# Kernel optimization log

Measured on AMD Instinct MI355X. Metric: run time of the kernel, lower is better.

## Reference

```python
import jax, jax.numpy as jnp
import numpy as np

B, S, D, H = 2, 2048, 1024, 16
HD = D // H                      # 64
NUM_ROPE_DIMS = 2
NF = HD // (2 * NUM_ROPE_DIMS)   # 16 freqs per rope dim -> total HD//2
FFN_H = 4 * D


def householder_matrix(vs):
    """Product of Householder reflections: Q = prod_i (I - 2 v_i v_i^T / ||v_i||^2)."""
    dim = vs.shape[-1]
    def step(Q, v):
        v = v[:, None]
        Q = Q - (2.0 / (jnp.sum(v * v) + 1e-8)) * (v @ (v.T @ Q))
        return Q, None
    Q, _ = jax.lax.scan(step, jnp.eye(dim, dtype=vs.dtype), vs)
    return Q


def rmsnorm(x):
    # torch.nn.RMSNorm(eps=None) uses dtype eps, no affine
    return x * jax.lax.rsqrt(jnp.mean(x * x, axis=-1, keepdims=True) + jnp.finfo(x.dtype).eps)


def setup_inputs() -> dict:
    key = jax.random.key(0)
    ks = jax.random.split(key, 8)
    x = jax.random.normal(ks[0], (B, S, D), jnp.float32)
    mask = jnp.tril(jnp.ones((S, S), dtype=bool))          # causal block mask
    qkv_w = jax.random.normal(ks[1], (3 * D, D), jnp.float32) * 0.02
    out_w = jax.random.normal(ks[2], (D, D), jnp.float32) * 0.02
    gate_w = jax.random.normal(ks[3], (D, D), jnp.float32) * 0.02
    gate_b = jnp.zeros((D,), jnp.float32)
    w12 = jax.random.normal(ks[4], (2 * FFN_H, D), jnp.float32) * 0.02
    w3 = jax.random.normal(ks[5], (D, FFN_H), jnp.float32) * 0.02
    hh_vs = jax.random.normal(ks[6], (HD // 2, HD), jnp.float32) * 0.02
    inv_freq = 1.0 / (10000.0 ** (jnp.arange(NF, dtype=jnp.float32) / NF))
    pos = jnp.arange(S, dtype=jnp.float32)
    rope_pos = jnp.stack([pos, pos], axis=-1)              # [S, num_rope_dims]
    return dict(x=x, mask=mask, qkv_w=qkv_w, out_w=out_w, gate_w=gate_w,
                gate_b=gate_b, w12=w12, w3=w3, hh_vs=hh_vs,
                inv_freq=inv_freq, rope_pos=rope_pos)


def reference(x, mask, qkv_w, out_w, gate_w, gate_b, w12, w3, hh_vs, inv_freq, rope_pos):
    Bs, Ss, Ds = x.shape
    resid = x
    xn = rmsnorm(x)
    qkv = xn @ qkv_w.T                                      # [B,S,3D]
    q, k, v = jnp.split(qkv, 3, axis=-1)
    q = q.reshape(Bs, Ss, H, HD).transpose(0, 2, 1, 3)      # [B,H,S,HD]
    k = k.reshape(Bs, Ss, H, HD).transpose(0, 2, 1, 3)
    v = v.reshape(Bs, Ss, H, HD).transpose(0, 2, 1, 3)

    # RnRoPE: rotate into canonical basis, apply RoPE, rotate back
    Q = householder_matrix(hh_vs)                           # [HD,HD]
    q = q @ Q.T
    k = k @ Q.T
    # geo_state.scale = 1.0
    full = jnp.einsum('sd,f->sdf', rope_pos, inv_freq).reshape(Ss, -1)  # [S, HD//2]
    half = HD // 2
    full = full[:, :half]
    emb = jnp.concatenate([full, full], axis=-1)            # [S, HD]
    cos, sin = jnp.cos(emb), jnp.sin(emb)

    def rot(t):
        t1, t2 = jnp.split(t, 2, axis=-1)
        return t * cos + jnp.concatenate([-t2, t1], axis=-1) * sin

    q = rot(q) @ Q
    k = rot(k) @ Q

    # block-masked attention (flex_attention default scale = 1/sqrt(HD))
    scores = jnp.einsum('bhsd,bhtd->bhst', q, k) / jnp.sqrt(jnp.asarray(HD, x.dtype))
    scores = jnp.where(mask, scores, -jnp.inf)
    attn = jax.nn.softmax(scores, axis=-1)
    o = jnp.einsum('bhst,bhtd->bhsd', attn, v)
    o = o.transpose(0, 2, 1, 3).reshape(Bs, Ss, Ds)
    o = o @ out_w.T
    gate = jax.nn.sigmoid(o @ gate_w.T + gate_b)
    x = resid + o * gate

    # SwiGLU FFN
    resid2 = x
    xn2 = rmsnorm(x)
    x12 = xn2 @ w12.T
    x1, x2 = jnp.split(x12, 2, axis=-1)
    ffn = (jax.nn.silu(x1) * x2) @ w3.T
    return resid2 + ffn
```

## Files before the change

kernel.cpp:

```cpp
#include <hip/hip_runtime.h>
#include <hip/hip_bf16.h>
#include <math.h>

constexpr int Bc = 2, Sc = 2048, Dc = 1024, Hc = 16, HDc = 64;
constexpr int D3 = 3 * Dc;

typedef __bf16 bf16x8 __attribute__((ext_vector_type(8)));
typedef float f32x4 __attribute__((ext_vector_type(4)));

__device__ __forceinline__ void gll16(const void* g, void* l) {
  __builtin_amdgcn_global_load_lds((const __attribute__((address_space(1))) unsigned int*)g,
                                   (__attribute__((address_space(3))) unsigned int*)l,
                                   16, 0, 0);
}

__device__ __forceinline__ unsigned short f2bf(float v) {
  __hip_bfloat16 h = __float2bfloat16(v);
  return *(unsigned short*)&h;
}
__device__ __forceinline__ float b2f(unsigned short u) {
  unsigned v = ((unsigned)u) << 16;
  return __uint_as_float(v);
}

#define SBAR() asm volatile("s_barrier" ::: "memory")

__global__ __launch_bounds__(256) void f2b_kernel(const float* __restrict__ in,
                                                  unsigned short* __restrict__ out) {
  int i = blockIdx.x * 256 + threadIdx.x;
  float4 v = ((const float4*)in)[i];
  ushort4 o;
  o.x = f2bf(v.x); o.y = f2bf(v.y); o.z = f2bf(v.z); o.w = f2bf(v.w);
  ((ushort4*)out)[i] = o;
}

__global__ __launch_bounds__(256) void w12i_kernel(const float* __restrict__ in,
                                                   unsigned short* __restrict__ out) {
  int r = blockIdx.x;
  int g = r >> 5, u = r & 31;
  int src = ((u < 16) ? 0 : 4096) + g * 16 + (u & 15);
  float4 v = ((const float4*)(in + (size_t)src * 1024))[threadIdx.x];
  ushort4 o;
  o.x = f2bf(v.x); o.y = f2bf(v.y); o.z = f2bf(v.z); o.w = f2bf(v.w);
  ((ushort4*)(out + (size_t)r * 1024))[threadIdx.x] = o;
}

__global__ __launch_bounds__(256) void rmsnorm_bf16_kernel(const float* __restrict__ in,
                                                           unsigned short* __restrict__ out) {
  int row = blockIdx.x;
  const float4* x4 = (const float4*)(in + (size_t)row * Dc);
  float4 v = x4[threadIdx.x];
  float s = v.x * v.x + v.y * v.y + v.z * v.z + v.w * v.w;
#pragma unroll
  for (int off = 1; off < 64; off <<= 1) s += __shfl_xor(s, off);
  __shared__ float wsum[4];
  if ((threadIdx.x & 63) == 0) wsum[threadIdx.x >> 6] = s;
  __syncthreads();
  float tot = wsum[0] + wsum[1] + wsum[2] + wsum[3];
  float r = rsqrtf(tot * (1.0f / Dc) + 1.1920928955078125e-07f);
  ushort4 o;
  o.x = f2bf(v.x * r); o.y = f2bf(v.y * r); o.z = f2bf(v.z * r); o.w = f2bf(v.w * r);
  ((ushort4*)(out + (size_t)row * Dc))[threadIdx.x] = o;
}

__global__ __launch_bounds__(64) void hh_kernel(const float* __restrict__ vs,
                                                float* __restrict__ Qout) {
  __shared__ float Qm[64][65];
  __shared__ float vsh[64];
  int t = threadIdx.x;
  for (int i = 0; i < 64; ++i) Qm[i][t] = (i == t) ? 1.0f : 0.0f;
  for (int it = 0; it < 32; ++it) {
    __syncthreads();
    vsh[t] = vs[it * 64 + t];
    __syncthreads();
    float nv = 0.0f;
    for (int i = 0; i < 64; ++i) nv += vsh[i] * vsh[i];
    float c = 2.0f / (nv + 1e-8f);
    float wj = 0.0f;
    for (int i = 0; i < 64; ++i) wj += vsh[i] * Qm[i][t];
    for (int i = 0; i < 64; ++i) Qm[i][t] -= c * vsh[i] * wj;
  }
  __syncthreads();
  for (int i = 0; i < 64; ++i) Qout[i * 64 + t] = Qm[i][t];
}

__global__ __launch_bounds__(256) void wqk_kernel(const float* __restrict__ W,
                                                  const float* __restrict__ Qm,
                                                  unsigned short* __restrict__ out) {
  int n = blockIdx.x;
  int r = n & 63;
  int base = n & ~63;
  int t = threadIdx.x;
  float a0 = 0, a1 = 0, a2 = 0, a3 = 0;
  const float4* Wp = (const float4*)(W + (size_t)base * 1024) + t;
#pragma unroll 8
  for (int e = 0; e < 64; ++e) {
    float q = Qm[r * 64 + e];
    float4 wv = Wp[(size_t)e * 256];
    a0 += q * wv.x; a1 += q * wv.y; a2 += q * wv.z; a3 += q * wv.w;
  }
  float sc = (n < 1024) ? 0.18033688f : 1.0f;
  ushort4 o;
  o.x = f2bf(a0 * sc); o.y = f2bf(a1 * sc); o.z = f2bf(a2 * sc); o.w = f2bf(a3 * sc);
  ((ushort4*)(out + (size_t)n * 1024))[t] = o;
}

__global__ __launch_bounds__(256) void rtab_kernel(const float* __restrict__ rope_pos,
                                                   const float* __restrict__ inv_freq,
                                                   float2* __restrict__ tab) {
  int id = blockIdx.x * 256 + threadIdx.x;
  int s = id >> 5, d = id & 31;
  float pos = rope_pos[s * 2 + (d >> 4)];
  float emb = pos * inv_freq[d & 15];
  tab[id] = make_float2(cosf(emb), sinf(emb));
}

__global__ __launch_bounds__(256) void rope_kernel(const unsigned short* __restrict__ qkv,
                                                   const float2* __restrict__ tab,
                                                   unsigned short* __restrict__ qb,
                                                   unsigned short* __restrict__ kb) {
  int t = threadIdx.x;
  int gid = blockIdx.x * 64 + (t >> 2);
  int sub = t & 3;
  int h = gid & 15;
  int which = (gid >> 4) & 1;
  int tok = gid >> 5;
  int s = tok & (Sc - 1), b = tok >> 11;
  const unsigned short* src = qkv + (size_t)tok * D3 + which * Dc + h * 64 + sub * 8;
  uint4 lov = *(const uint4*)src;
  uint4 hiv = *(const uint4*)(src + 32);
  const unsigned short* lp = (const unsigned short*)&lov;
  const unsigned short* hp = (const unsigned short*)&hiv;
  unsigned short olo[8], ohi[8];
  const float2* tp = tab + s * 32 + sub * 8;
#pragma unroll
  for (int i = 0; i < 8; ++i) {
    float2 cs = tp[i];
    float lo = b2f(lp[i]), hi = b2f(hp[i]);
    olo[i] = f2bf(lo * cs.x - hi * cs.y);
    ohi[i] = f2bf(hi * cs.x + lo * cs.y);
  }
  unsigned short* dst = (which ? kb : qb) + ((size_t)((b * Hc + h) * Sc + s)) * 64 + sub * 8;
  *(uint4*)dst = *(uint4*)olo;
  *(uint4*)(dst + 32) = *(uint4*)ohi;
}

__global__ __launch_bounds__(256) void vt_kernel(const unsigned short* __restrict__ qkv,
                                                 unsigned short* __restrict__ vtb) {
  __shared__ unsigned short tile[64 * 72];
  int st = blockIdx.x;
  int bh = blockIdx.y;
  int b = bh >> 4, h = bh & 15;
  int t = threadIdx.x;
  int srow = t >> 2, c16 = (t & 3) * 16;
  const unsigned short* src =
      qkv + (size_t)(b * Sc + st * 64 + srow) * D3 + 2 * Dc + h * 64 + c16;
  uint4 a0 = *(const uint4*)src;
  uint4 a1 = *(const uint4*)(src + 8);
  *(uint4*)(tile + srow * 72 + c16) = a0;
  *(uint4*)(tile + srow * 72 + c16 + 8) = a1;
  __syncthreads();
  int d = t >> 2, sch = (t & 3) * 16;
  unsigned short tmp[16];
#pragma unroll
  for (int i = 0; i < 16; ++i) tmp[i] = tile[(sch + i) * 72 + d];
  unsigned short* dst = vtb + ((size_t)(bh * 64 + d)) * Sc + st * 64 + sch;
  *(uint4*)dst = *(uint4*)tmp;
  *(uint4*)(dst + 8) = *(uint4*)(tmp + 8);
}

template <int MODE>
__global__ __launch_bounds__(512, 1) void mgemm8p(const unsigned short* __restrict__ A,
                                                  const unsigned short* __restrict__ B,
                                                  unsigned short* __restrict__ C,
                                                  int M, int N, int K) {
  __shared__ unsigned short lds[65536];
  const int t = threadIdx.x;
  const int lane = t & 63;
  const int wave = t >> 6;
  const int wr = wave >> 2, wc = wave & 3;
  const int l15 = lane & 15, l4 = lane >> 4;
  const int gx = gridDim.x;
  const int nwg = gx * gridDim.y;
  const int id = blockIdx.y * gx + blockIdx.x;
  const int swz = (id & 7) * (nwg >> 3) + (id >> 3);
  const int m0 = (swz / gx) * 256;
  const int n0 = (swz % gx) * 256;
  const int NT = K >> 6;
  const int sko = (((t & 3) ^ ((t >> 3) & 3)) * 8);
  const unsigned short* ag0 = A + (size_t)(m0 + (t >> 2)) * K + sko;
  const unsigned short* ag1 = ag0 + (size_t)128 * K;
  const unsigned short* bg0 = B + (size_t)(n0 + (t >> 2)) * K + sko;
  const unsigned short* bg1 = bg0 + (size_t)128 * K;
  const int t8 = t * 8;
  const int ks = (l4 ^ ((l15 >> 1) & 3)) * 8;
  gll16(ag0, lds + t8);
  gll16(ag1, lds + 4096 + t8);
  gll16(bg0, lds + 32768 + t8);
  gll16(bg1, lds + 32768 + 4096 + t8);
  gll16(ag0 + 32, lds + 8192 + t8);
  gll16(ag1 + 32, lds + 8192 + 4096 + t8);
  gll16(bg0 + 32, lds + 32768 + 8192 + t8);
  gll16(bg1 + 32, lds + 32768 + 8192 + 4096 + t8);
  asm volatile("s_waitcnt vmcnt(4)" ::: "memory");
  SBAR();
  f32x4 acc[8][4] = {};
  for (int kt = 0; kt < NT; ++kt) {
    const int cur = (kt & 1) << 14;
    const int nxt = cur ^ 16384;
    const int kof = ((kt + 1 < NT) ? (kt + 1) : kt) << 6;
    const unsigned short* Ap = lds + cur;
    const unsigned short* Bp = lds + 32768 + cur;
    bf16x8 a[8], b0, b1;
#pragma unroll
    for (int i = 0; i < 8; ++i)
      a[i] = *(const bf16x8*)(Ap + (wr * 128 + i * 16 + l15) * 32 + ks);
    b0 = *(const bf16x8*)(Bp + (wc * 64 + l15) * 32 + ks);
    b1 = *(const bf16x8*)(Bp + (wc * 64 + 16 + l15) * 32 + ks);
    gll16(ag0 + kof, lds + nxt + t8);
    gll16(ag1 + kof, lds + nxt + 4096 + t8);
    SBAR();
    __builtin_amdgcn_s_setprio(1);
#pragma unroll
    for (int i = 0; i < 8; ++i) {
      acc[i][0] = __builtin_amdgcn_mfma_f32_16x16x32_bf16(a[i], b0, acc[i][0], 0, 0, 0);
      acc[i][1] = __builtin_amdgcn_mfma_f32_16x16x32_bf16(a[i], b1, acc[i][1], 0, 0, 0);
    }
    __builtin_amdgcn_s_setprio(0);
    SBAR();
    b0 = *(const bf16x8*)(Bp + (wc * 64 + 32 + l15) * 32 + ks);
    b1 = *(const bf16x8*)(Bp + (wc * 64 + 48 + l15) * 32 + ks);
    gll16(bg0 + kof, lds + 32768 + nxt + t8);
    gll16(bg1 + kof, lds + 32768 + nxt + 4096 + t8);
    asm volatile("s_waitcnt vmcnt(4)" ::: "memory");
    SBAR();
    __builtin_amdgcn_s_setprio(1);
#pragma unroll
    for (int i = 0; i < 8; ++i) {
      acc[i][2] = __builtin_amdgcn_mfma_f32_16x16x32_bf16(a[i], b0, acc[i][2], 0, 0, 0);
      acc[i][3] = __builtin_amdgcn_mfma_f32_16x16x32_bf16(a[i], b1, acc[i][3], 0, 0, 0);
    }
    __builtin_amdgcn_s_setprio(0);
    SBAR();
#pragma unroll
    for (int i = 0; i < 8; ++i)
      a[i] = *(const bf16x8*)(Ap + 8192 + (wr * 128 + i * 16 + l15) * 32 + ks);
    b0 = *(const bf16x8*)(Bp + 8192 + (wc * 64 + l15) * 32 + ks);
    b1 = *(const bf16x8*)(Bp + 8192 + (wc * 64 + 16 + l15) * 32 + ks);
    gll16(ag0 + kof + 32, lds + nxt + 8192 + t8);
    gll16(ag1 + kof + 32, lds + nxt + 8192 + 4096 + t8);
    SBAR();
    __builtin_amdgcn_s_setprio(1);
#pragma unroll
    for (int i = 0; i < 8; ++i) {
      acc[i][0] = __builtin_amdgcn_mfma_f32_16x16x32_bf16(a[i], b0, acc[i][0], 0, 0, 0);
      acc[i][1] = __builtin_amdgcn_mfma_f32_16x16x32_bf16(a[i], b1, acc[i][1], 0, 0, 0);
    }
    __builtin_amdgcn_s_setprio(0);
    SBAR();
    b0 = *(const bf16x8*)(Bp + 8192 + (wc * 64 + 32 + l15) * 32 + ks);
    b1 = *(const bf16x8*)(Bp + 8192 + (wc * 64 + 48 + l15) * 32 + ks);
    gll16(bg0 + kof + 32, lds + 32768 + nxt + 8192 + t8);
    gll16(bg1 + kof + 32, lds + 32768 + nxt + 8192 + 4096 + t8);
    asm volatile("s_waitcnt vmcnt(4)" ::: "memory");
    SBAR();
    __builtin_amdgcn_s_setprio(1);
#pragma unroll
    for (int i = 0; i < 8; ++i) {
      acc[i][2] = __builtin_amdgcn_mfma_f32_16x16x32_bf16(a[i], b0, acc[i][2], 0, 0, 0);
      acc[i][3] = __builtin_amdgcn_mfma_f32_16x16x32_bf16(a[i], b1, acc[i][3], 0, 0, 0);
    }
    __builtin_amdgcn_s_setprio(0);
    SBAR();
  }
  asm volatile("s_waitcnt vmcnt(0)" ::: "memory");
  const int r0 = m0 + wr * 128 + l4 * 4;
  if (MODE == 0) {
    const int c0 = n0 + wc * 64 + l15;
#pragma unroll
    for (int i = 0; i < 8; ++i)
#pragma unroll
      for (int j = 0; j < 4; ++j)
#pragma unroll
        for (int r = 0; r < 4; ++r)
          C[(size_t)(r0 + i * 16 + r) * N + c0 + j * 16] = f2bf(acc[i][j][r]);
  } else {
    const int nc = N >> 1;
    const int c0 = (n0 >> 1) + wc * 32 + l15;
#pragma unroll
    for (int i = 0; i < 8; ++i)
#pragma unroll
      for (int p = 0; p < 2; ++p)
#pragma unroll
        for (int r = 0; r < 4; ++r) {
          float v = acc[i][2 * p][r];
          float sv = v / (1.0f + expf(-v));
          C[(size_t)(r0 + i * 16 + r) * nc + c0 + p * 16] = f2bf(sv * acc[i][2 * p + 1][r]);
        }
  }
}

template <int MODE>
__global__ __launch_bounds__(256, 3) void mgemm64(const unsigned short* __restrict__ A,
                                                  const unsigned short* __restrict__ W,
                                                  const float* __restrict__ R,
                                                  const float* __restrict__ R2,
                                                  const float* __restrict__ bias,
                                                  void* __restrict__ Cout,
                                                  void* __restrict__ Cout2,
                                                  int M, int N, int K) {
  __shared__ unsigned short As[2048];
  __shared__ unsigned short Bs[4096];
  const int t = threadIdx.x;
  const int lane = t & 63;
  const int wave = t >> 6;
  const int wr = wave >> 1, wc = wave & 1;
  const int m0 = blockIdx.y * 64, n0 = blockIdx.x * 128;
  f32x4 acc[2][4] = {};
  const int srow = t >> 2;
  const int sch = (t & 3) * 8;
  const unsigned short* Ag = A + (size_t)(m0 + srow) * K + sch;
  const unsigned short* Wg = W + (size_t)(n0 + srow) * K + sch;
  const size_t rstep = (size_t)64 * K;
  const int frow = lane & 15;
  const int fk = (lane >> 4) * 8;
  for (int k0 = 0; k0 < K; k0 += 32) {
    __syncthreads();
    gll16(Ag + k0, As + t * 8);
    gll16(Wg + k0, Bs + t * 8);
    gll16(Wg + k0 + rstep, Bs + 2048 + t * 8);
    __syncthreads();
    bf16x8 af[2], bq[4];
#pragma unroll
    for (int i = 0; i < 2; ++i)
      af[i] = *(const bf16x8*)(As + (wr * 32 + i * 16 + frow) * 32 + fk);
#pragma unroll
    for (int j = 0; j < 4; ++j)
      bq[j] = *(const bf16x8*)(Bs + (wc * 64 + j * 16 + frow) * 32 + fk);
#pragma unroll
    for (int i = 0; i < 2; ++i)
#pragma unroll
      for (int j = 0; j < 4; ++j)
        acc[i][j] = __builtin_amdgcn_mfma_f32_16x16x32_bf16(af[i], bq[j], acc[i][j], 0, 0, 0);
  }
  const int crow = wr * 32 + (lane >> 4) * 4;
  const int ccol = wc * 64 + (lane & 15);
#pragma unroll
  for (int i = 0; i < 2; ++i) {
#pragma unroll
    for (int j = 0; j < 4; ++j) {
#pragma unroll
      for (int r = 0; r < 4; ++r) {
        int row = m0 + crow + i * 16 + r;
        int col = n0 + ccol + j * 16;
        float v = acc[i][j][r];
        size_t off = (size_t)row * N + col;
        if (MODE == 2) {
          ((float*)Cout)[off] = v + R[off];
        } else if (MODE == 4) {
          ((float*)Cout)[off] = v;
          ((unsigned short*)Cout2)[off] = f2bf(v);
        } else {
          float g = v + bias[col];
          float sg = 1.0f / (1.0f + expf(-g));
          ((float*)Cout)[off] = R[off] + R2[off] * sg;
        }
      }
    }
  }
}

__global__ __launch_bounds__(256) void mattn(const unsigned short* __restrict__ qb,
                                             const unsigned short* __restrict__ kb,
                                             const unsigned short* __restrict__ vtb,
                                             unsigned short* __restrict__ out) {
  __shared__ unsigned short Qs[8192];
  __shared__ unsigned short Ks[4096];
  __shared__ unsigned short Vts[4096];
  __shared__ unsigned short Ps[4 * 16 * 72];
  const int qt = gridDim.x - 1 - blockIdx.x;
  const int bh = blockIdx.y;
  const int b = bh >> 4, h = bh & 15;
  const int t = threadIdx.x, lane = t & 63, w = t >> 6;
  const int l15 = lane & 15, l4 = lane >> 4;
  const unsigned short* qbase = qb + ((size_t)bh * Sc + qt * 128) * 64;
  const unsigned short* kbase = kb + (size_t)bh * Sc * 64;
  const unsigned short* vbase = vtb + (size_t)bh * 64 * Sc;
#pragma unroll
  for (int i = 0; i < 4; ++i) {
    int idx = t + i * 256;
    int r = idx >> 3;
    int cg = (idx & 7) ^ (r & 7);
    gll16(qbase + (size_t)r * 64 + cg * 8, Qs + idx * 8);
  }
  bf16x8 qf[2][2];
  f32x4 oacc[2][4] = {};
  float lrow[2][4] = {};
  unsigned short* pw = Ps + w * 16 * 72;
  const int ktmax = 2 * qt + 1;
  for (int kt = 0; kt <= ktmax; ++kt) {
    __syncthreads();
    {
      int r = t >> 3;
      int cg = (t & 7) ^ (r & 7);
      gll16(kbase + (size_t)(kt * 64 + r) * 64 + cg * 8, Ks + t * 8);
      gll16(kbase + (size_t)(kt * 64 + r + 32) * 64 + cg * 8, Ks + 2048 + t * 8);
      gll16(vbase + (size_t)r * Sc + kt * 64 + cg * 8, Vts + t * 8);
      gll16(vbase + (size_t)(r + 32) * Sc + kt * 64 + cg * 8, Vts + 2048 + t * 8);
    }
    __syncthreads();
    if (kt == 0) {
#pragma unroll
      for (int ch = 0; ch < 2; ++ch) {
        int qrow = ch * 64 + w * 16 + l15;
#pragma unroll
        for (int kc = 0; kc < 2; ++kc)
          qf[ch][kc] = *(const bf16x8*)(Qs + qrow * 64 + (((kc * 4 + l4) ^ (l15 & 7)) * 8));
      }
    }
    const bool actA = (kt <= 2 * qt);
    f32x4 sc[2][4] = {};
#pragma unroll
    for (int kc = 0; kc < 2; ++kc) {
      bf16x8 kf[4];
#pragma unroll
      for (int j = 0; j < 4; ++j)
        kf[j] = *(const bf16x8*)(Ks + (j * 16 + l15) * 64 + (((kc * 4 + l4) ^ (l15 & 7)) * 8));
      if (actA) {
#pragma unroll
        for (int j = 0; j < 4; ++j)
          sc[0][j] = __builtin_amdgcn_mfma_f32_16x16x32_bf16(qf[0][kc], kf[j], sc[0][j], 0, 0, 0);
      }
#pragma unroll
      for (int j = 0; j < 4; ++j)
        sc[1][j] = __builtin_amdgcn_mfma_f32_16x16x32_bf16(qf[1][kc], kf[j], sc[1][j], 0, 0, 0);
    }
    const int rl = w * 16 + l4 * 4;
    if (kt == 2 * qt) {
#pragma unroll
      for (int j = 0; j < 4; ++j)
#pragma unroll
        for (int r = 0; r < 4; ++r)
          if (j * 16 + l15 > rl + r) sc[0][j][r] = -INFINITY;
    }
    if (kt == ktmax) {
#pragma unroll
      for (int j = 0; j < 4; ++j)
#pragma unroll
        for (int r = 0; r < 4; ++r)
          if (j * 16 + l15 > rl + r) sc[1][j][r] = -INFINITY;
    }
    bf16x8 vf[2][4];
#pragma unroll
    for (int kc = 0; kc < 2; ++kc)
#pragma unroll
      for (int j = 0; j < 4; ++j)
        vf[kc][j] = *(const bf16x8*)(Vts + (j * 16 + l15) * 64 + (((kc * 4 + l4) ^ (l15 & 7)) * 8));
#pragma unroll
    for (int ch = 0; ch < 2; ++ch) {
      if (ch == 0 && !actA) continue;
#pragma unroll
      for (int j = 0; j < 4; ++j)
#pragma unroll
        for (int r = 0; r < 4; ++r) {
          float p = exp2f(sc[ch][j][r]);
          lrow[ch][r] += p;
          pw[(l4 * 4 + r) * 72 + j * 16 + l15] = f2bf(p);
        }
      __asm__ __volatile__("s_waitcnt lgkmcnt(0)" ::: "memory");
#pragma unroll
      for (int kc = 0; kc < 2; ++kc) {
        bf16x8 pf = *(const bf16x8*)(pw + l15 * 72 + kc * 32 + l4 * 8);
#pragma unroll
        for (int j = 0; j < 4; ++j)
          oacc[ch][j] = __builtin_amdgcn_mfma_f32_16x16x32_bf16(pf, vf[kc][j], oacc[ch][j], 0, 0, 0);
      }
    }
  }
#pragma unroll
  for (int ch = 0; ch < 2; ++ch) {
#pragma unroll
    for (int r = 0; r < 4; ++r) {
      float s = lrow[ch][r];
      s += __shfl_xor(s, 1);
      s += __shfl_xor(s, 2);
      s += __shfl_xor(s, 4);
      s += __shfl_xor(s, 8);
      float inv = 1.0f / s;
#pragma unroll
      for (int j = 0; j < 4; ++j) {
        int srow = qt * 128 + ch * 64 + w * 16 + l4 * 4 + r;
        out[((size_t)(b * Sc + srow)) * Dc + h * 64 + j * 16 + l15] =
            f2bf(oacc[ch][j][r] * inv);
      }
    }
  }
}

extern "C" void kernel_launch(void* const* d_in, const int* in_sizes, int n_in,
                              void* d_out, int out_size, void* d_ws, size_t ws_size,
                              hipStream_t stream) {
  const float* x        = (const float*)d_in[0];
  const float* qkv_w    = (const float*)d_in[2];
  const float* out_w    = (const float*)d_in[3];
  const float* gate_w   = (const float*)d_in[4];
  const float* gate_b   = (const float*)d_in[5];
  const float* w12      = (const float*)d_in[6];
  const float* w3       = (const float*)d_in[7];
  const float* hh_vs    = (const float*)d_in[8];
  const float* inv_freq = (const float*)d_in[9];
  const float* rope_pos = (const float*)d_in[10];
  char* ws = (char*)d_ws;
  unsigned short* woutb  = (unsigned short*)(ws + 0);
  float2*         rtab   = (float2*)(ws + 2097152);
  unsigned short* wqkvb  = (unsigned short*)(ws + 4194304);
  unsigned short* attnb  = (unsigned short*)(ws + 4194304);
  float*          xmid   = (float*)(ws + 0);
  unsigned short* slotB  = (unsigned short*)(ws + 16777216);
  float*          oproj  = (float*)(ws + 25165824);
  unsigned short* w12b   = (unsigned short*)(ws + 25165824);
  unsigned short* wgateb = (unsigned short*)(ws + 41943040);
  unsigned short* w3b    = (unsigned short*)(ws + 41943040);
  unsigned short* qkvb   = (unsigned short*)(ws + 58720256);
  unsigned short* hbufb  = (unsigned short*)(ws + 58720256);
  unsigned short* qb     = (unsigned short*)(ws + 83886080);
  unsigned short* oprojb = (unsigned short*)(ws + 83886080);
  unsigned short* kb     = (unsigned short*)(ws + 92274688);
  unsigned short* vtb    = (unsigned short*)(ws + 100663296);
  float*          Qb     = (float*)(ws + 109051904);
  float* outp = (float*)d_out;

  hh_kernel<<<1, 64, 0, stream>>>(hh_vs, Qb);
  rtab_kernel<<<256, 256, 0, stream>>>(rope_pos, inv_freq, rtab);
  wqk_kernel<<<2048, 256, 0, stream>>>(qkv_w, Qb, wqkvb);
  f2b_kernel<<<1024, 256, 0, stream>>>(qkv_w + 2048 * 1024,
                                       wqkvb + 2048 * 1024);
  f2b_kernel<<<1024, 256, 0, stream>>>(out_w, woutb);
  f2b_kernel<<<1024, 256, 0, stream>>>(gate_w, wgateb);
  rmsnorm_bf16_kernel<<<4096, 256, 0, stream>>>(x, slotB);
  mgemm8p<0><<<dim3(12, 16), 512, 0, stream>>>(slotB, wqkvb, qkvb, 4096, 3072, 1024);
  rope_kernel<<<2048, 256, 0, stream>>>(qkvb, rtab, qb, kb);
  vt_kernel<<<dim3(32, 32), 256, 0, stream>>>(qkvb, vtb);
  mattn<<<dim3(16, 32), 256, 0, stream>>>(qb, kb, vtb, attnb);
  mgemm64<4><<<dim3(8, 64), 256, 0, stream>>>(attnb, woutb, nullptr, nullptr, nullptr,
                                              oproj, oprojb, 4096, 1024, 1024);
  mgemm64<5><<<dim3(8, 64), 256, 0, stream>>>(oprojb, wgateb, x, oproj, gate_b,
                                              xmid, nullptr, 4096, 1024, 1024);
  w12i_kernel<<<8192, 256, 0, stream>>>(w12, w12b);
  f2b_kernel<<<4096, 256, 0, stream>>>(w3, w3b);
  rmsnorm_bf16_kernel<<<4096, 256, 0, stream>>>(xmid, slotB);
  mgemm8p<1><<<dim3(32, 16), 512, 0, stream>>>(slotB, w12b, hbufb, 4096, 8192, 1024);
  mgemm64<2><<<dim3(8, 64), 256, 0, stream>>>(hbufb, w3b, xmid, nullptr, nullptr,
                                              outp, nullptr, 4096, 1024, 4096);
}
```

Before: 560.0 us.

## Double-buffer K/V tiles in attention kernel and raise MFMA wave priority

The attention kernel now keeps two LDS buffers for K and V and issues the async global-to-LDS loads for the next key tile before computing on the current one. It waits with a partial vmcnt so only the current tile must have landed, which overlaps memory latency with MFMA work. It also raises wave priority around the MFMA blocks via s_setprio. The cost is double the K/V LDS footprint, a redundant reload on the last iteration, and correctness that depends on the vmcnt counting matching the four outstanding loads.

```diff
diff --git a/kernel.cpp b/kernel.cpp
--- a/kernel.cpp
+++ b/kernel.cpp
@@ -375,8 +375,8 @@
                                              const unsigned short* __restrict__ vtb,
                                              unsigned short* __restrict__ out) {
   __shared__ unsigned short Qs[8192];
-  __shared__ unsigned short Ks[4096];
-  __shared__ unsigned short Vts[4096];
+  __shared__ unsigned short Ks[2][4096];
+  __shared__ unsigned short Vts[2][4096];
   __shared__ unsigned short Ps[4 * 16 * 72];
   const int qt = gridDim.x - 1 - blockIdx.x;
   const int bh = blockIdx.y;
@@ -393,22 +393,26 @@
     int cg = (idx & 7) ^ (r & 7);
     gll16(qbase + (size_t)r * 64 + cg * 8, Qs + idx * 8);
   }
+  const int sr = t >> 3;
+  const int scg = (t & 7) ^ (sr & 7);
+  gll16(kbase + (size_t)sr * 64 + scg * 8, Ks[0] + t * 8);
+  gll16(kbase + (size_t)(sr + 32) * 64 + scg * 8, Ks[0] + 2048 + t * 8);
+  gll16(vbase + (size_t)sr * Sc + scg * 8, Vts[0] + t * 8);
+  gll16(vbase + (size_t)(sr + 32) * Sc + scg * 8, Vts[0] + 2048 + t * 8);
   bf16x8 qf[2][2];
   f32x4 oacc[2][4] = {};
   float lrow[2][4] = {};
   unsigned short* pw = Ps + w * 16 * 72;
   const int ktmax = 2 * qt + 1;
   for (int kt = 0; kt <= ktmax; ++kt) {
-    __syncthreads();
-    {
-      int r = t >> 3;
-      int cg = (t & 7) ^ (r & 7);
-      gll16(kbase + (size_t)(kt * 64 + r) * 64 + cg * 8, Ks + t * 8);
-      gll16(kbase + (size_t)(kt * 64 + r + 32) * 64 + cg * 8, Ks + 2048 + t * 8);
-      gll16(vbase + (size_t)r * Sc + kt * 64 + cg * 8, Vts + t * 8);
-      gll16(vbase + (size_t)(r + 32) * Sc + kt * 64 + cg * 8, Vts + 2048 + t * 8);
-    }
-    __syncthreads();
+    const int cur = kt & 1;
+    const int ktn = (kt < ktmax) ? kt + 1 : kt;
+    gll16(kbase + (size_t)(ktn * 64 + sr) * 64 + scg * 8, Ks[cur ^ 1] + t * 8);
+    gll16(kbase + (size_t)(ktn * 64 + sr + 32) * 64 + scg * 8, Ks[cur ^ 1] + 2048 + t * 8);
+    gll16(vbase + (size_t)sr * Sc + ktn * 64 + scg * 8, Vts[cur ^ 1] + t * 8);
+    gll16(vbase + (size_t)(sr + 32) * Sc + ktn * 64 + scg * 8, Vts[cur ^ 1] + 2048 + t * 8);
+    asm volatile("s_waitcnt vmcnt(4)" ::: "memory");
+    SBAR();
     if (kt == 0) {
 #pragma unroll
       for (int ch = 0; ch < 2; ++ch) {
@@ -425,7 +429,8 @@
       bf16x8 kf[4];
 #pragma unroll
       for (int j = 0; j < 4; ++j)
-        kf[j] = *(const bf16x8*)(Ks + (j * 16 + l15) * 64 + (((kc * 4 + l4) ^ (l15 & 7)) * 8));
+        kf[j] = *(const bf16x8*)(Ks[cur] + (j * 16 + l15) * 64 + (((kc * 4 + l4) ^ (l15 & 7)) * 8));
+      __builtin_amdgcn_s_setprio(1);
       if (actA) {
 #pragma unroll
         for (int j = 0; j < 4; ++j)
@@ -434,6 +439,7 @@
 #pragma unroll
       for (int j = 0; j < 4; ++j)
         sc[1][j] = __builtin_amdgcn_mfma_f32_16x16x32_bf16(qf[1][kc], kf[j], sc[1][j], 0, 0, 0);
+      __builtin_amdgcn_s_setprio(0);
     }
     const int rl = w * 16 + l4 * 4;
     if (kt == 2 * qt) {
@@ -455,7 +461,7 @@
     for (int kc = 0; kc < 2; ++kc)
 #pragma unroll
       for (int j = 0; j < 4; ++j)
-        vf[kc][j] = *(const bf16x8*)(Vts + (j * 16 + l15) * 64 + (((kc * 4 + l4) ^ (l15 & 7)) * 8));
+        vf[kc][j] = *(const bf16x8*)(Vts[cur] + (j * 16 + l15) * 64 + (((kc * 4 + l4) ^ (l15 & 7)) * 8));
 #pragma unroll
     for (int ch = 0; ch < 2; ++ch) {
       if (ch == 0 && !actA) continue;
@@ -468,6 +474,7 @@
           pw[(l4 * 4 + r) * 72 + j * 16 + l15] = f2bf(p);
         }
       __asm__ __volatile__("s_waitcnt lgkmcnt(0)" ::: "memory");
+      __builtin_amdgcn_s_setprio(1);
 #pragma unroll
       for (int kc = 0; kc < 2; ++kc) {
         bf16x8 pf = *(const bf16x8*)(pw + l15 * 72 + kc * 32 + l4 * 8);
@@ -475,8 +482,11 @@
         for (int j = 0; j < 4; ++j)
           oacc[ch][j] = __builtin_amdgcn_mfma_f32_16x16x32_bf16(pf, vf[kc][j], oacc[ch][j], 0, 0, 0);
       }
-    }
-  }
+      __builtin_amdgcn_s_setprio(0);
+    }
+    SBAR();
+  }
+  asm volatile("s_waitcnt vmcnt(0)" ::: "memory");
 #pragma unroll
   for (int ch = 0; ch < 2; ++ch) {
 #pragma unroll
```

Result: no change. 569.4 us (+1.7%).
